# Kernel optimization log

Measured on AMD Instinct MI355X. Metric: run time of the kernel, lower is better.

Reference implementation:

```python
import jax, jax.numpy as jnp
import numpy as np

T, B, I, H, L = 512, 32, 512, 1024, 2


def setup_inputs() -> dict:
    key = jax.random.key(0)
    ks = jax.random.split(key, 10)
    std = 1.0 / np.sqrt(H)
    u = lambda k, shape: jax.random.uniform(k, shape, jnp.float32, -std, std)
    return {
        "x": jax.random.normal(ks[0], (T, B, I), jnp.float32),
        "Wxh0": u(ks[1], (4 * H, I)),
        "bxh0": u(ks[2], (4 * H,)),
        "Whh0": u(ks[3], (4 * H, H)),
        "bhh0": u(ks[4], (4 * H,)),
        "Wxh1": u(ks[5], (4 * H, H)),
        "bxh1": u(ks[6], (4 * H,)),
        "Whh1": u(ks[7], (4 * H, H)),
        "bhh1": u(ks[8], (4 * H,)),
    }


def _lstm_layer(x_seq, Wxh, bxh, Whh, bhh):
    # x_seq: (T, B, D_in). Precompute input projections for all timesteps.
    xg = jnp.einsum('tbi,gi->tbg', x_seq, Wxh) + bxh  # (T, B, 4H)
    h0 = jnp.zeros((x_seq.shape[1], H), x_seq.dtype)
    c0 = jnp.zeros_like(h0)

    def step(carry, xg_t):
        h, c = carry
        gates = xg_t + h @ Whh.T + bhh  # (B, 4H)
        i_g, f_g, g_g, o_g = jnp.split(gates, 4, axis=-1)
        c_new = jax.nn.sigmoid(f_g) * c + jax.nn.sigmoid(i_g) * jnp.tanh(g_g)
        h_new = jax.nn.sigmoid(o_g) * jnp.tanh(c_new)
        return (h_new, c_new), h_new

    (h_T, c_T), hs = jax.lax.scan(step, (h0, c0), xg)
    return hs, h_T, c_T  # hs: (T, B, H)


def reference(x, Wxh0, bxh0, Whh0, bhh0, Wxh1, bxh1, Whh1, bhh1):
    # Layer 0 consumes raw input; layer 1 consumes layer-0 hidden sequence.
    # Processing layer-by-layer is mathematically identical to the original
    # interleaved (t, layer) loop for a stacked unidirectional LSTM.
    hs0, h0T, c0T = _lstm_layer(x, Wxh0, bxh0, Whh0, bhh0)
    hs1, h1T, c1T = _lstm_layer(hs0, Wxh1, bxh1, Whh1, bhh1)
    output = hs1  # (T, B, H): hidden of last layer at each timestep
    h_n = jnp.stack([h0T, h1T])  # (L, B, H)
    c_n = jnp.stack([c0T, c1T])
    return output, h_n, c_n
```

## Files before the change

### kernel.cpp

```cpp
#include <hip/hip_runtime.h>


typedef unsigned short u16;
typedef __attribute__((ext_vector_type(8))) __bf16 bf16x8;
typedef __attribute__((ext_vector_type(8))) u16 u16x8;
typedef __attribute__((ext_vector_type(4))) float f32x4;
typedef __attribute__((ext_vector_type(2))) float f32x2;
typedef __attribute__((ext_vector_type(4))) int i32x4;
typedef __attribute__((ext_vector_type(4))) unsigned int u32x4;

#define HN_OFF 16777216
#define CN_OFF 16842752

__device__ __forceinline__ u16 f2bf(float f) {
  unsigned u = __builtin_bit_cast(unsigned, f);
  u += 0x7FFFu + ((u >> 16) & 1u);
  return (u16)(u >> 16);
}
__device__ __forceinline__ float sgm(float x) { return 1.f / (1.f + __expf(-x)); }
__device__ __forceinline__ float tnh(float x) { return 2.f / (1.f + __expf(-2.f * x)) - 1.f; }

__device__ __forceinline__ bf16x8 ld16(const u16* p) {
  u32x4 v = *reinterpret_cast<const u32x4*>(p);
  return __builtin_bit_cast(bf16x8, v);
}
__device__ __forceinline__ bf16x8 lds16(const char* p) {
  u32x4 v = *reinterpret_cast<const u32x4*>(p);
  return __builtin_bit_cast(bf16x8, v);
}
__device__ __forceinline__ f32x4 mfma16(bf16x8 a, bf16x8 b, f32x4 c) {
  return __builtin_amdgcn_mfma_f32_16x16x32_bf16(a, b, c, 0, 0, 0);
}

__device__ __forceinline__ void pollge(const int* flags, int lane, int s) {
  const int* p = flags + (lane << 2);
  for (;;) {
    i32x4 f;
    asm volatile("global_load_dwordx4 %0, %1, off sc0 sc1\n\ts_waitcnt vmcnt(0)"
                 : "=v"(f) : "v"(p) : "memory");
    if (__all((f[0] >= s) & (f[1] >= s) & (f[2] >= s) & (f[3] >= s))) break;
  }
}

template <int C0, int C1>
__device__ __forceinline__ void chunks_h0(const u16* __restrict__ A,
                                          const char* w0, const char* w1, int lane,
                                          f32x4& p0, f32x4& p1, f32x4& q0, f32x4& q1) {
  const int r = lane & 15, kq = (lane >> 4) * 8, swz = (r & 7) << 4;
#pragma unroll
  for (int c = C0; c < C1; ++c) {
    const u16* ap = A + r * 1024 + c * 32 + kq;
    bf16x8 a0 = ld16(ap);
    bf16x8 a1 = ld16(ap + 16 * 1024);
    bf16x8 b0 = lds16(w0 + r * 3072 + ((c * 64 + kq * 2) ^ swz));
    bf16x8 b1 = lds16(w1 + r * 4096 + (((c + 32) * 64 + kq * 2) ^ swz));
    p0 = mfma16(a0, b0, p0);  p1 = mfma16(a1, b0, p1);
    q0 = mfma16(a0, b1, q0);  q1 = mfma16(a1, b1, q1);
  }
}
template <int C0, int C1>
__device__ __forceinline__ void chunks_h1(const u16* __restrict__ A,
                                          const char* w1, int lane,
                                          f32x4& p0, f32x4& p1) {
  const int r = lane & 15, kq = (lane >> 4) * 8, swz = (r & 7) << 4;
#pragma unroll
  for (int c = C0; c < C1; ++c) {
    const u16* ap = A + r * 1024 + c * 32 + kq;
    bf16x8 a0 = ld16(ap);
    bf16x8 a1 = ld16(ap + 16 * 1024);
    bf16x8 bw = lds16(w1 + r * 4096 + ((c * 64 + kq * 2) ^ swz));
    p0 = mfma16(a0, bw, p0);  p1 = mfma16(a1, bw, p1);
  }
}
template <int C0, int C1>
__device__ __forceinline__ void chunks_x(const u16* __restrict__ A,
                                         const char* w0, int lane,
                                         f32x4& q0, f32x4& q1) {
  const int r = lane & 15, kq = (lane >> 4) * 8, swz = (r & 7) << 4;
#pragma unroll
  for (int c = C0; c < C1; ++c) {
    const u16* ap = A + r * 512 + c * 32 + kq;
    bf16x8 a0 = ld16(ap);
    bf16x8 a1 = ld16(ap + 16 * 512);
    bf16x8 bw = lds16(w0 + r * 3072 + (((c + 32) * 64 + kq * 2) ^ swz));
    q0 = mfma16(a0, bw, q0);  q1 = mfma16(a1, bw, q1);
  }
}

__global__ __launch_bounds__(512, 2) void lstm_fused(
    const u16* __restrict__ xbf,
    const float* __restrict__ Whh0, const float* __restrict__ Wxh0,
    const float* __restrict__ Whh1, const float* __restrict__ Wxh1,
    const float* __restrict__ bxh0, const float* __restrict__ bhh0,
    const float* __restrict__ bxh1, const float* __restrict__ bhh1,
    u16* __restrict__ h0seq, u16* __restrict__ h1seq,
    int* __restrict__ flag0, int* __restrict__ flag1,
    float* __restrict__ out) {
  extern __shared__ char smem[];
  const char* w0 = smem;
  const char* w1 = smem + 49152;
  auto part = reinterpret_cast<float(*)[32][18]>(smem + 114688);
  float* bias0 = reinterpret_cast<float*>(smem + 151552);
  float* bias1 = reinterpret_cast<float*>(smem + 151616);
  volatile int* go = reinterpret_cast<volatile int*>(smem + 151680);

  const int tid = threadIdx.x;
  const int wg = blockIdx.x;
  const int wid = tid >> 6, lane = tid & 63;

  if (tid == 0) { go[0] = 0; go[1] = 0; }
  for (int g = tid; g < 3072; g += 512) {
    int n = g / 192, gi = g % 192, kc = gi * 8;
    int gr = ((n >> 2) << 10) + (wg << 2) + (n & 3);
    const float* src = (kc < 1024) ? (Whh0 + gr * 1024 + kc) : (Wxh0 + gr * 512 + (kc - 1024));
    f32x4 lo = *reinterpret_cast<const f32x4*>(src);
    f32x4 hi = *reinterpret_cast<const f32x4*>(src + 4);
    u16x8 o;
    o[0]=f2bf(lo[0]); o[1]=f2bf(lo[1]); o[2]=f2bf(lo[2]); o[3]=f2bf(lo[3]);
    o[4]=f2bf(hi[0]); o[5]=f2bf(hi[1]); o[6]=f2bf(hi[2]); o[7]=f2bf(hi[3]);
    *reinterpret_cast<u16x8*>(smem + n * 3072 + ((gi * 16) ^ ((n & 7) << 4))) = o;
  }
  for (int g = tid; g < 4096; g += 512) {
    int n = g / 256, gi = g % 256, kc = gi * 8;
    int gr = ((n >> 2) << 10) + (wg << 2) + (n & 3);
    const float* src = (kc < 1024) ? (Whh1 + gr * 1024 + kc) : (Wxh1 + gr * 1024 + (kc - 1024));
    f32x4 lo = *reinterpret_cast<const f32x4*>(src);
    f32x4 hi = *reinterpret_cast<const f32x4*>(src + 4);
    u16x8 o;
    o[0]=f2bf(lo[0]); o[1]=f2bf(lo[1]); o[2]=f2bf(lo[2]); o[3]=f2bf(lo[3]);
    o[4]=f2bf(hi[0]); o[5]=f2bf(hi[1]); o[6]=f2bf(hi[2]); o[7]=f2bf(hi[3]);
    *reinterpret_cast<u16x8*>(smem + 49152 + n * 4096 + ((gi * 16) ^ ((n & 7) << 4))) = o;
  }
  if (tid < 16) {
    int gr = ((tid >> 2) << 10) + (wg << 2) + (tid & 3);
    bias0[tid] = bxh0[gr] + bhh0[gr];
    bias1[tid] = bxh1[gr] + bhh1[gr];
  }
  __syncthreads();

  float c0a = 0.f, c0b = 0.f, c1a = 0.f, c1b = 0.f;
  const int bg = lane >> 1, jjb = (lane & 1) << 1;
  const int colb = (wg << 2) + jjb;

  for (int s = 0; s <= 512; ++s) {
    const u16* h0slot = h0seq + s * 32768;
    const u16* h1prev = h1seq + (s - 1) * 32768;
    f32x4 p0 = {0,0,0,0}, p1 = {0,0,0,0}, q0 = {0,0,0,0}, q1 = {0,0,0,0};

    if (wid < 4) {
      if (s >= 1) {
        if (wid == 0) {
          pollge(flag0, lane, s);
          if (lane == 0) go[0] = s;
        } else {
          while (go[0] < s) __builtin_amdgcn_s_sleep(1);
        }
      }
      if      (wid == 0) chunks_h0<0,  8 >(h0slot, w0, w1, lane, p0, p1, q0, q1);
      else if (wid == 1) chunks_h0<8,  16>(h0slot, w0, w1, lane, p0, p1, q0, q1);
      else if (wid == 2) chunks_h0<16, 24>(h0slot, w0, w1, lane, p0, p1, q0, q1);
      else               chunks_h0<24, 32>(h0slot, w0, w1, lane, p0, p1, q0, q1);
    } else {
      const u16* xbt = xbf + s * 16384;
      if      (wid == 4) chunks_x<0,  4 >(xbt, w0, lane, q0, q1);
      else if (wid == 5) chunks_x<4,  8 >(xbt, w0, lane, q0, q1);
      else if (wid == 6) chunks_x<8,  12>(xbt, w0, lane, q0, q1);
      else               chunks_x<12, 16>(xbt, w0, lane, q0, q1);
      if (s >= 2) {
        if (wid == 4) {
          pollge(flag1, lane, s);
          if (lane == 0) go[1] = s;
        } else {
          while (go[1] < s) __builtin_amdgcn_s_sleep(1);
        }
      }
      if      (wid == 4) chunks_h1<0,  8 >(h1prev, w1, lane, p0, p1);
      else if (wid == 5) chunks_h1<8,  16>(h1prev, w1, lane, p0, p1);
      else if (wid == 6) chunks_h1<16, 24>(h1prev, w1, lane, p0, p1);
      else               chunks_h1<24, 32>(h1prev, w1, lane, p0, p1);
    }

    {
      const int n = lane & 15, br = (lane >> 4) * 4;
#pragma unroll
      for (int j = 0; j < 4; ++j) {
        part[wid][br + j][n]      = p0[j];
        part[wid][br + j + 16][n] = p1[j];
        part[8 + wid][br + j][n]      = q0[j];
        part[8 + wid][br + j + 16][n] = q1[j];
      }
    }
    __syncthreads();

    if (wid == 0) {
      if (s < 512) {
        float v[4][2];
#pragma unroll
        for (int gi = 0; gi < 4; ++gi) {
          const int n = (gi << 2) + jjb;
          float s0 = bias0[n], s1 = bias0[n + 1];
#pragma unroll
          for (int p = 0; p < 4; ++p) {
            f32x2 a = *reinterpret_cast<const f32x2*>(&part[p][bg][n]);
            f32x2 b = *reinterpret_cast<const f32x2*>(&part[12 + p][bg][n]);
            s0 += a[0] + b[0];  s1 += a[1] + b[1];
          }
          v[gi][0] = s0; v[gi][1] = s1;
        }
        c0a = sgm(v[1][0]) * c0a + sgm(v[0][0]) * tnh(v[2][0]);
        c0b = sgm(v[1][1]) * c0b + sgm(v[0][1]) * tnh(v[2][1]);
        const float ha = sgm(v[3][0]) * tnh(c0a), hb = sgm(v[3][1]) * tnh(c0b);
        unsigned pk = (unsigned)f2bf(ha) | ((unsigned)f2bf(hb) << 16);
        u16* hp = h0seq + (s + 1) * 32768 + bg * 1024 + colb;
        asm volatile("global_store_dword %0, %1, off sc0 sc1" :: "v"(hp), "v"(pk) : "memory");
        if (s == 511) {
          *reinterpret_cast<f32x2*>(out + HN_OFF + bg * 1024 + colb) = f32x2{ha, hb};
          *reinterpret_cast<f32x2*>(out + CN_OFF + bg * 1024 + colb) = f32x2{c0a, c0b};
        }
        asm volatile("s_waitcnt vmcnt(0)" ::: "memory");
        if (lane == 0) {
          int* fp = flag0 + wg;  int fv = s + 1;
          asm volatile("global_store_dword %0, %1, off sc0 sc1" :: "v"(fp), "v"(fv) : "memory");
        }
      }
    } else if (wid == 4) {
      if (s >= 1) {
        float v[4][2];
#pragma unroll
        for (int gi = 0; gi < 4; ++gi) {
          const int n = (gi << 2) + jjb;
          float s0 = bias1[n], s1 = bias1[n + 1];
#pragma unroll
          for (int p = 4; p < 12; ++p) {
            f32x2 a = *reinterpret_cast<const f32x2*>(&part[p][bg][n]);
            s0 += a[0];  s1 += a[1];
          }
          v[gi][0] = s0; v[gi][1] = s1;
        }
        c1a = sgm(v[1][0]) * c1a + sgm(v[0][0]) * tnh(v[2][0]);
        c1b = sgm(v[1][1]) * c1b + sgm(v[0][1]) * tnh(v[2][1]);
        const float ha = sgm(v[3][0]) * tnh(c1a), hb = sgm(v[3][1]) * tnh(c1b);
        unsigned pk = (unsigned)f2bf(ha) | ((unsigned)f2bf(hb) << 16);
        u16* hp = h1seq + s * 32768 + bg * 1024 + colb;
        asm volatile("global_store_dword %0, %1, off sc0 sc1" :: "v"(hp), "v"(pk) : "memory");
        const int t1 = s - 1;
        *reinterpret_cast<f32x2*>(out + t1 * 32768 + bg * 1024 + colb) = f32x2{ha, hb};
        if (t1 == 511) {
          *reinterpret_cast<f32x2*>(out + HN_OFF + 32768 + bg * 1024 + colb) = f32x2{ha, hb};
          *reinterpret_cast<f32x2*>(out + CN_OFF + 32768 + bg * 1024 + colb) = f32x2{c1a, c1b};
        }
        asm volatile("s_waitcnt vmcnt(0)" ::: "memory");
        if (lane == 0) {
          int* fp = flag1 + wg;  int fv = s + 1;
          asm volatile("global_store_dword %0, %1, off sc0 sc1" :: "v"(fp), "v"(fv) : "memory");
        }
      }
    }

    if (s == 512) break;
    __syncthreads();
  }
}

__global__ void cvt_bf16(const float* __restrict__ s, u16* __restrict__ d, int n) {
  int i = (blockIdx.x * blockDim.x + threadIdx.x) * 4;
  const int stride = gridDim.x * blockDim.x * 4;
  typedef __attribute__((ext_vector_type(4))) u16 u16x4;
  for (; i < n; i += stride) {
    f32x4 v = *reinterpret_cast<const f32x4*>(s + i);
    u16x4 o;
    o[0] = f2bf(v[0]); o[1] = f2bf(v[1]); o[2] = f2bf(v[2]); o[3] = f2bf(v[3]);
    *reinterpret_cast<u16x4*>(d + i) = o;
  }
}

extern "C" void kernel_launch(void* const* d_in, const int* in_sizes, int n_in,
                              void* d_out, int out_size, void* d_ws, size_t ws_size,
                              hipStream_t stream) {
  const float* x    = (const float*)d_in[0];
  const float* Wxh0 = (const float*)d_in[1];
  const float* bxh0 = (const float*)d_in[2];
  const float* Whh0 = (const float*)d_in[3];
  const float* bhh0 = (const float*)d_in[4];
  const float* Wxh1 = (const float*)d_in[5];
  const float* bxh1 = (const float*)d_in[6];
  const float* Whh1 = (const float*)d_in[7];
  const float* bhh1 = (const float*)d_in[8];
  char* ws = (char*)d_ws;
  u16* xbf   = (u16*)(ws);
  u16* h0seq = (u16*)(ws + 16777216);
  u16* h1seq = (u16*)(ws + 50397184);
  int* flag0 = (int*)(ws + 84017152);
  int* flag1 = (int*)(ws + 84018176);

  cvt_bf16<<<2048, 256, 0, stream>>>(x, xbf, 512 * 32 * 512);
  (void)hipMemsetAsync(h0seq, 0, 65536, stream);
  (void)hipMemsetAsync(h1seq, 0, 65536, stream);
  (void)hipMemsetAsync(flag0, 0, 2048, stream);

  (void)hipFuncSetAttribute(reinterpret_cast<const void*>(lstm_fused),
                            hipFuncAttributeMaxDynamicSharedMemorySize, 151744);
  lstm_fused<<<dim3(256), dim3(512), 151744, stream>>>(
      xbf, Whh0, Wxh0, Whh1, Wxh1, bxh0, bhh0, bxh1, bhh1,
      h0seq, h1seq, flag0, flag1, (float*)d_out);
}
```

Measured before the change: 3.437 ms.

## Merge per-layer grid flags into one epoch barrier with a single master poller

Replaces the two per-step flag polls (layer-0 waves and layer-1 waves each polling all 256 workgroup flags) with one combined barrier. Workgroup 0 polls both flag arrays and publishes an epoch word, and every other workgroup spins on that single dword. The input-projection MFMAs are hoisted ahead of the barrier so they overlap the wait. Cell-update duties move to waves 1 and 5, flag stores are issued before the output writes, and the trailing intra-block sync is dropped because the grid barrier now orders reuse of the shared partials. This cuts polling traffic on the flag lines, but it adds an extra hop of latency through the master workgroup and couples the two layers' progress at every step.

```diff
diff --git a/kernel.cpp b/kernel.cpp
--- a/kernel.cpp
+++ b/kernel.cpp
@@ -32,13 +32,25 @@
   return __builtin_amdgcn_mfma_f32_16x16x32_bf16(a, b, c, 0, 0, 0);
 }
 
-__device__ __forceinline__ void pollge(const int* flags, int lane, int s) {
-  const int* p = flags + (lane << 2);
+__device__ __forceinline__ void poll_flags(const int* f, int lane, int s) {
+  const int* p0 = f + (lane << 2);
+  const int* p1 = f + 256 + (lane << 2);
   for (;;) {
-    i32x4 f;
-    asm volatile("global_load_dwordx4 %0, %1, off sc0 sc1\n\ts_waitcnt vmcnt(0)"
-                 : "=v"(f) : "v"(p) : "memory");
-    if (__all((f[0] >= s) & (f[1] >= s) & (f[2] >= s) & (f[3] >= s))) break;
+    i32x4 a, b;
+    asm volatile("global_load_dwordx4 %0, %2, off sc0 sc1\n\t"
+                 "global_load_dwordx4 %1, %3, off sc0 sc1\n\t"
+                 "s_waitcnt vmcnt(0)"
+                 : "=v"(a), "=v"(b) : "v"(p0), "v"(p1) : "memory");
+    if (__all((a[0] >= s) & (a[1] >= s) & (a[2] >= s) & (a[3] >= s) &
+              (b[0] >= s) & (b[1] >= s) & (b[2] >= s) & (b[3] >= s))) break;
+  }
+}
+__device__ __forceinline__ void poll_epoch(const int* ep, int s) {
+  for (;;) {
+    int e;
+    asm volatile("global_load_dword %0, %1, off sc0 sc1\n\ts_waitcnt vmcnt(0)"
+                 : "=v"(e) : "v"(ep) : "memory");
+    if (e >= s) break;
   }
 }
 
@@ -94,7 +106,7 @@
     const float* __restrict__ bxh0, const float* __restrict__ bhh0,
     const float* __restrict__ bxh1, const float* __restrict__ bhh1,
     u16* __restrict__ h0seq, u16* __restrict__ h1seq,
-    int* __restrict__ flag0, int* __restrict__ flag1,
+    int* __restrict__ flagbase,
     float* __restrict__ out) {
   extern __shared__ char smem[];
   const char* w0 = smem;
@@ -104,11 +116,15 @@
   float* bias1 = reinterpret_cast<float*>(smem + 151616);
   volatile int* go = reinterpret_cast<volatile int*>(smem + 151680);
 
+  int* flag0 = flagbase;
+  int* flag1 = flagbase + 256;
+  int* epoch = flagbase + 512;
+
   const int tid = threadIdx.x;
   const int wg = blockIdx.x;
   const int wid = tid >> 6, lane = tid & 63;
 
-  if (tid == 0) { go[0] = 0; go[1] = 0; }
+  if (tid == 0) go[0] = 0;
   for (int g = tid; g < 3072; g += 512) {
     int n = g / 192, gi = g % 192, kc = gi * 8;
     int gr = ((n >> 2) << 10) + (wg << 2) + (n & 3);
@@ -147,33 +163,38 @@
     const u16* h1prev = h1seq + (s - 1) * 32768;
     f32x4 p0 = {0,0,0,0}, p1 = {0,0,0,0}, q0 = {0,0,0,0}, q1 = {0,0,0,0};
 
-    if (wid < 4) {
-      if (s >= 1) {
-        if (wid == 0) {
-          pollge(flag0, lane, s);
-          if (lane == 0) go[0] = s;
-        } else {
-          while (go[0] < s) __builtin_amdgcn_s_sleep(1);
-        }
-      }
-      if      (wid == 0) chunks_h0<0,  8 >(h0slot, w0, w1, lane, p0, p1, q0, q1);
-      else if (wid == 1) chunks_h0<8,  16>(h0slot, w0, w1, lane, p0, p1, q0, q1);
-      else if (wid == 2) chunks_h0<16, 24>(h0slot, w0, w1, lane, p0, p1, q0, q1);
-      else               chunks_h0<24, 32>(h0slot, w0, w1, lane, p0, p1, q0, q1);
-    } else {
+    if (wid >= 4 && s < 512) {
       const u16* xbt = xbf + s * 16384;
       if      (wid == 4) chunks_x<0,  4 >(xbt, w0, lane, q0, q1);
       else if (wid == 5) chunks_x<4,  8 >(xbt, w0, lane, q0, q1);
       else if (wid == 6) chunks_x<8,  12>(xbt, w0, lane, q0, q1);
       else               chunks_x<12, 16>(xbt, w0, lane, q0, q1);
-      if (s >= 2) {
-        if (wid == 4) {
-          pollge(flag1, lane, s);
-          if (lane == 0) go[1] = s;
+    }
+
+    if (s >= 1) {
+      if (wid == 0) {
+        if (wg == 0) {
+          poll_flags(flag0, lane, s);
+          if (lane == 0) {
+            int sv = s;
+            asm volatile("global_store_dword %0, %1, off sc0 sc1"
+                         :: "v"(epoch), "v"(sv) : "memory");
+          }
         } else {
-          while (go[1] < s) __builtin_amdgcn_s_sleep(1);
-        }
+          poll_epoch(epoch, s);
+        }
+        if (lane == 0) go[0] = s;
+      } else {
+        while (go[0] < s) __builtin_amdgcn_s_sleep(1);
       }
+    }
+
+    if (wid < 4) {
+      if      (wid == 0) chunks_h0<0,  8 >(h0slot, w0, w1, lane, p0, p1, q0, q1);
+      else if (wid == 1) chunks_h0<8,  16>(h0slot, w0, w1, lane, p0, p1, q0, q1);
+      else if (wid == 2) chunks_h0<16, 24>(h0slot, w0, w1, lane, p0, p1, q0, q1);
+      else               chunks_h0<24, 32>(h0slot, w0, w1, lane, p0, p1, q0, q1);
+    } else if (s >= 1) {
       if      (wid == 4) chunks_h1<0,  8 >(h1prev, w1, lane, p0, p1);
       else if (wid == 5) chunks_h1<8,  16>(h1prev, w1, lane, p0, p1);
       else if (wid == 6) chunks_h1<16, 24>(h1prev, w1, lane, p0, p1);
@@ -184,15 +205,15 @@
       const int n = lane & 15, br = (lane >> 4) * 4;
 #pragma unroll
       for (int j = 0; j < 4; ++j) {
-        part[wid][br + j][n]      = p0[j];
-        part[wid][br + j + 16][n] = p1[j];
+        part[wid][br + j][n]          = p0[j];
+        part[wid][br + j + 16][n]     = p1[j];
         part[8 + wid][br + j][n]      = q0[j];
         part[8 + wid][br + j + 16][n] = q1[j];
       }
     }
     __syncthreads();
 
-    if (wid == 0) {
+    if (wid == 1) {
       if (s < 512) {
         float v[4][2];
 #pragma unroll
@@ -213,17 +234,17 @@
         unsigned pk = (unsigned)f2bf(ha) | ((unsigned)f2bf(hb) << 16);
         u16* hp = h0seq + (s + 1) * 32768 + bg * 1024 + colb;
         asm volatile("global_store_dword %0, %1, off sc0 sc1" :: "v"(hp), "v"(pk) : "memory");
-        if (s == 511) {
-          *reinterpret_cast<f32x2*>(out + HN_OFF + bg * 1024 + colb) = f32x2{ha, hb};
-          *reinterpret_cast<f32x2*>(out + CN_OFF + bg * 1024 + colb) = f32x2{c0a, c0b};
-        }
         asm volatile("s_waitcnt vmcnt(0)" ::: "memory");
         if (lane == 0) {
           int* fp = flag0 + wg;  int fv = s + 1;
           asm volatile("global_store_dword %0, %1, off sc0 sc1" :: "v"(fp), "v"(fv) : "memory");
         }
+        if (s == 511) {
+          *reinterpret_cast<f32x2*>(out + HN_OFF + bg * 1024 + colb) = f32x2{ha, hb};
+          *reinterpret_cast<f32x2*>(out + CN_OFF + bg * 1024 + colb) = f32x2{c0a, c0b};
+        }
       }
-    } else if (wid == 4) {
+    } else if (wid == 5) {
       if (s >= 1) {
         float v[4][2];
 #pragma unroll
@@ -243,22 +264,22 @@
         unsigned pk = (unsigned)f2bf(ha) | ((unsigned)f2bf(hb) << 16);
         u16* hp = h1seq + s * 32768 + bg * 1024 + colb;
         asm volatile("global_store_dword %0, %1, off sc0 sc1" :: "v"(hp), "v"(pk) : "memory");
+        asm volatile("s_waitcnt vmcnt(0)" ::: "memory");
+        if (lane == 0) {
+          int* fp = flag1 + wg;  int fv = s + 1;
+          asm volatile("global_store_dword %0, %1, off sc0 sc1" :: "v"(fp), "v"(fv) : "memory");
+        }
         const int t1 = s - 1;
         *reinterpret_cast<f32x2*>(out + t1 * 32768 + bg * 1024 + colb) = f32x2{ha, hb};
         if (t1 == 511) {
           *reinterpret_cast<f32x2*>(out + HN_OFF + 32768 + bg * 1024 + colb) = f32x2{ha, hb};
           *reinterpret_cast<f32x2*>(out + CN_OFF + 32768 + bg * 1024 + colb) = f32x2{c1a, c1b};
         }
-        asm volatile("s_waitcnt vmcnt(0)" ::: "memory");
-        if (lane == 0) {
-          int* fp = flag1 + wg;  int fv = s + 1;
-          asm volatile("global_store_dword %0, %1, off sc0 sc1" :: "v"(fp), "v"(fv) : "memory");
-        }
+      } else if (lane == 0) {
+        int* fp = flag1 + wg;  int fv = 1;
+        asm volatile("global_store_dword %0, %1, off sc0 sc1" :: "v"(fp), "v"(fv) : "memory");
       }
     }
-
-    if (s == 512) break;
-    __syncthreads();
   }
 }
 
@@ -287,20 +308,19 @@
   const float* Whh1 = (const float*)d_in[7];
   const float* bhh1 = (const float*)d_in[8];
   char* ws = (char*)d_ws;
-  u16* xbf   = (u16*)(ws);
-  u16* h0seq = (u16*)(ws + 16777216);
-  u16* h1seq = (u16*)(ws + 50397184);
-  int* flag0 = (int*)(ws + 84017152);
-  int* flag1 = (int*)(ws + 84018176);
+  u16* xbf      = (u16*)(ws);
+  u16* h0seq    = (u16*)(ws + 16777216);
+  u16* h1seq    = (u16*)(ws + 50397184);
+  int* flagbase = (int*)(ws + 84017152);
 
   cvt_bf16<<<2048, 256, 0, stream>>>(x, xbf, 512 * 32 * 512);
   (void)hipMemsetAsync(h0seq, 0, 65536, stream);
   (void)hipMemsetAsync(h1seq, 0, 65536, stream);
-  (void)hipMemsetAsync(flag0, 0, 2048, stream);
+  (void)hipMemsetAsync(flagbase, 0, 4096, stream);
 
   (void)hipFuncSetAttribute(reinterpret_cast<const void*>(lstm_fused),
                             hipFuncAttributeMaxDynamicSharedMemorySize, 151744);
   lstm_fused<<<dim3(256), dim3(512), 151744, stream>>>(
       xbf, Whh0, Wxh0, Whh1, Wxh1, bxh0, bhh0, bxh1, bhh1,
-      h0seq, h1seq, flag0, flag1, (float*)d_out);
-}
+      h0seq, h1seq, flagbase, (float*)d_out);
+}
```

Result: slower. 3.517 ms (+2.3%).

## Replace flag polling with sentinel-filled hidden-state buffers and prefetch x projections

Applied to the files above, without the earlier changes.

Each step's hidden-state buffer is pre-filled with a 0xFFFFFFFF sentinel, and consumer waves poll the data itself (16 dwordx4 loads per lane, retried until no sentinel remains). This removes the separate flag arrays, the store-then-wait-then-flag round trip on the producer side, and the LDS 'go' broadcast. The x-input projection for step s+1 is now computed by spare waves after the gate stage of step s, taking it off the critical path, and gate finalisation moves to waves 1 and 5. The price is a 64 MB sentinel memset per call and wider polling loads, and correctness relies on real bf16 outputs never matching the sentinel.

```diff
diff --git a/kernel.cpp b/kernel.cpp
--- a/kernel.cpp
+++ b/kernel.cpp
@@ -6,11 +6,11 @@
 typedef __attribute__((ext_vector_type(8))) u16 u16x8;
 typedef __attribute__((ext_vector_type(4))) float f32x4;
 typedef __attribute__((ext_vector_type(2))) float f32x2;
-typedef __attribute__((ext_vector_type(4))) int i32x4;
 typedef __attribute__((ext_vector_type(4))) unsigned int u32x4;
 
 #define HN_OFF 16777216
 #define CN_OFF 16842752
+#define SENTU 0xFFFFFFFFu
 
 __device__ __forceinline__ u16 f2bf(float f) {
   unsigned u = __builtin_bit_cast(unsigned, f);
@@ -32,46 +32,46 @@
   return __builtin_amdgcn_mfma_f32_16x16x32_bf16(a, b, c, 0, 0, 0);
 }
 
-__device__ __forceinline__ void pollge(const int* flags, int lane, int s) {
-  const int* p = flags + (lane << 2);
-  for (;;) {
-    i32x4 f;
-    asm volatile("global_load_dwordx4 %0, %1, off sc0 sc1\n\ts_waitcnt vmcnt(0)"
-                 : "=v"(f) : "v"(p) : "memory");
-    if (__all((f[0] >= s) & (f[1] >= s) & (f[2] >= s) & (f[3] >= s))) break;
-  }
-}
-
-template <int C0, int C1>
-__device__ __forceinline__ void chunks_h0(const u16* __restrict__ A,
-                                          const char* w0, const char* w1, int lane,
-                                          f32x4& p0, f32x4& p1, f32x4& q0, f32x4& q1) {
-  const int r = lane & 15, kq = (lane >> 4) * 8, swz = (r & 7) << 4;
-#pragma unroll
-  for (int c = C0; c < C1; ++c) {
-    const u16* ap = A + r * 1024 + c * 32 + kq;
-    bf16x8 a0 = ld16(ap);
-    bf16x8 a1 = ld16(ap + 16 * 1024);
-    bf16x8 b0 = lds16(w0 + r * 3072 + ((c * 64 + kq * 2) ^ swz));
-    bf16x8 b1 = lds16(w1 + r * 4096 + (((c + 32) * 64 + kq * 2) ^ swz));
-    p0 = mfma16(a0, b0, p0);  p1 = mfma16(a1, b0, p1);
-    q0 = mfma16(a0, b1, q0);  q1 = mfma16(a1, b1, q1);
-  }
-}
-template <int C0, int C1>
-__device__ __forceinline__ void chunks_h1(const u16* __restrict__ A,
-                                          const char* w1, int lane,
-                                          f32x4& p0, f32x4& p1) {
-  const int r = lane & 15, kq = (lane >> 4) * 8, swz = (r & 7) << 4;
-#pragma unroll
-  for (int c = C0; c < C1; ++c) {
-    const u16* ap = A + r * 1024 + c * 32 + kq;
-    bf16x8 a0 = ld16(ap);
-    bf16x8 a1 = ld16(ap + 16 * 1024);
-    bf16x8 bw = lds16(w1 + r * 4096 + ((c * 64 + kq * 2) ^ swz));
-    p0 = mfma16(a0, bw, p0);  p1 = mfma16(a1, bw, p1);
-  }
-}
+#define LD8A(a,b,c,d_,e,f,g,h,off,bs)                                   \
+  asm volatile("global_load_dwordx4 %0, %8, %9 offset:0 sc0 sc1\n\t"    \
+               "global_load_dwordx4 %1, %8, %9 offset:64 sc0 sc1\n\t"   \
+               "global_load_dwordx4 %2, %8, %9 offset:128 sc0 sc1\n\t"  \
+               "global_load_dwordx4 %3, %8, %9 offset:192 sc0 sc1\n\t"  \
+               "global_load_dwordx4 %4, %8, %9 offset:256 sc0 sc1\n\t"  \
+               "global_load_dwordx4 %5, %8, %9 offset:320 sc0 sc1\n\t"  \
+               "global_load_dwordx4 %6, %8, %9 offset:384 sc0 sc1\n\t"  \
+               "global_load_dwordx4 %7, %8, %9 offset:448 sc0 sc1"      \
+               : "=&v"(a), "=&v"(b), "=&v"(c), "=&v"(d_), "=&v"(e),     \
+                 "=&v"(f), "=&v"(g), "=&v"(h)                           \
+               : "v"(off), "s"(bs) : "memory")
+
+#define DECL16 u32x4 d0,d1,d2,d3,d4,d5,d6,d7,d8,d9,d10,d11,d12,d13,d14,d15
+#define CHK(v) (((v)[0]==SENTU)|((v)[1]==SENTU)|((v)[2]==SENTU)|((v)[3]==SENTU))
+#define RETRY16(bs,o0,o1)                                                   \
+  for (;;) {                                                                \
+    LD8A(d0,d1,d2,d3,d4,d5,d6,d7,(o0),(bs));                                \
+    LD8A(d8,d9,d10,d11,d12,d13,d14,d15,(o1),(bs));                          \
+    asm volatile("s_waitcnt vmcnt(0)" ::: "memory");                        \
+    __builtin_amdgcn_sched_barrier(0);                                      \
+    unsigned bad = CHK(d0)|CHK(d1)|CHK(d2)|CHK(d3)|CHK(d4)|CHK(d5)|CHK(d6)  \
+                 |CHK(d7)|CHK(d8)|CHK(d9)|CHK(d10)|CHK(d11)|CHK(d12)        \
+                 |CHK(d13)|CHK(d14)|CHK(d15);                               \
+    if (!__any(bad)) break;                                                 \
+    __builtin_amdgcn_s_sleep(1);                                            \
+  }
+
+#define MM_L0(di,dj,c) {                                                    \
+    bf16x8 b0 = lds16(w0 + r*3072 + (((c)*64 + kq2) ^ swz));                \
+    bf16x8 b1 = lds16(w1 + r*4096 + ((((c)+32)*64 + kq2) ^ swz));           \
+    bf16x8 a0 = __builtin_bit_cast(bf16x8, di);                             \
+    bf16x8 a1 = __builtin_bit_cast(bf16x8, dj);                             \
+    p0 = mfma16(a0,b0,p0);  p1 = mfma16(a1,b0,p1);                          \
+    qa = mfma16(a0,b1,qa);  qb = mfma16(a1,b1,qb); }
+#define MM_L1(di,dj,c) {                                                    \
+    bf16x8 bw = lds16(w1 + r*4096 + (((c)*64 + kq2) ^ swz));                \
+    p0 = mfma16(__builtin_bit_cast(bf16x8, di), bw, p0);                    \
+    p1 = mfma16(__builtin_bit_cast(bf16x8, dj), bw, p1); }
+
 template <int C0, int C1>
 __device__ __forceinline__ void chunks_x(const u16* __restrict__ A,
                                          const char* w0, int lane,
@@ -94,7 +94,6 @@
     const float* __restrict__ bxh0, const float* __restrict__ bhh0,
     const float* __restrict__ bxh1, const float* __restrict__ bhh1,
     u16* __restrict__ h0seq, u16* __restrict__ h1seq,
-    int* __restrict__ flag0, int* __restrict__ flag1,
     float* __restrict__ out) {
   extern __shared__ char smem[];
   const char* w0 = smem;
@@ -102,13 +101,12 @@
   auto part = reinterpret_cast<float(*)[32][18]>(smem + 114688);
   float* bias0 = reinterpret_cast<float*>(smem + 151552);
   float* bias1 = reinterpret_cast<float*>(smem + 151616);
-  volatile int* go = reinterpret_cast<volatile int*>(smem + 151680);
 
   const int tid = threadIdx.x;
   const int wg = blockIdx.x;
   const int wid = tid >> 6, lane = tid & 63;
-
-  if (tid == 0) { go[0] = 0; go[1] = 0; }
+  const int r = lane & 15, kq2 = ((lane >> 4) << 3) * 2, swz = (r & 7) << 4;
+
   for (int g = tid; g < 3072; g += 512) {
     int n = g / 192, gi = g % 192, kc = gi * 8;
     int gr = ((n >> 2) << 10) + (wg << 2) + (n & 3);
@@ -142,57 +140,53 @@
   const int bg = lane >> 1, jjb = (lane & 1) << 1;
   const int colb = (wg << 2) + jjb;
 
+  f32x4 xq0 = {0,0,0,0}, xq1 = {0,0,0,0};
+  if      (wid == 4) chunks_x<0, 6 >(xbf, w0, lane, xq0, xq1);
+  else if (wid == 6) chunks_x<6, 11>(xbf, w0, lane, xq0, xq1);
+  else if (wid == 7) chunks_x<11,16>(xbf, w0, lane, xq0, xq1);
+
   for (int s = 0; s <= 512; ++s) {
-    const u16* h0slot = h0seq + s * 32768;
-    const u16* h1prev = h1seq + (s - 1) * 32768;
-    f32x4 p0 = {0,0,0,0}, p1 = {0,0,0,0}, q0 = {0,0,0,0}, q1 = {0,0,0,0};
+    f32x4 p0 = {0,0,0,0}, p1 = {0,0,0,0}, qa = {0,0,0,0}, qb = {0,0,0,0};
 
     if (wid < 4) {
-      if (s >= 1) {
-        if (wid == 0) {
-          pollge(flag0, lane, s);
-          if (lane == 0) go[0] = s;
-        } else {
-          while (go[0] < s) __builtin_amdgcn_s_sleep(1);
-        }
-      }
-      if      (wid == 0) chunks_h0<0,  8 >(h0slot, w0, w1, lane, p0, p1, q0, q1);
-      else if (wid == 1) chunks_h0<8,  16>(h0slot, w0, w1, lane, p0, p1, q0, q1);
-      else if (wid == 2) chunks_h0<16, 24>(h0slot, w0, w1, lane, p0, p1, q0, q1);
-      else               chunks_h0<24, 32>(h0slot, w0, w1, lane, p0, p1, q0, q1);
-    } else {
-      const u16* xbt = xbf + s * 16384;
-      if      (wid == 4) chunks_x<0,  4 >(xbt, w0, lane, q0, q1);
-      else if (wid == 5) chunks_x<4,  8 >(xbt, w0, lane, q0, q1);
-      else if (wid == 6) chunks_x<8,  12>(xbt, w0, lane, q0, q1);
-      else               chunks_x<12, 16>(xbt, w0, lane, q0, q1);
-      if (s >= 2) {
-        if (wid == 4) {
-          pollge(flag1, lane, s);
-          if (lane == 0) go[1] = s;
-        } else {
-          while (go[1] < s) __builtin_amdgcn_s_sleep(1);
-        }
-      }
-      if      (wid == 4) chunks_h1<0,  8 >(h1prev, w1, lane, p0, p1);
-      else if (wid == 5) chunks_h1<8,  16>(h1prev, w1, lane, p0, p1);
-      else if (wid == 6) chunks_h1<16, 24>(h1prev, w1, lane, p0, p1);
-      else               chunks_h1<24, 32>(h1prev, w1, lane, p0, p1);
+      const u16* hb = h0seq + (size_t)s * 32768;
+      const int off0 = r * 2048 + wid * 512 + kq2;
+      const int off1 = off0 + 32768;
+      DECL16;
+      RETRY16(hb, off0, off1);
+      const int c0 = wid * 8;
+      MM_L0(d0, d8,  c0 + 0); MM_L0(d1, d9,  c0 + 1);
+      MM_L0(d2, d10, c0 + 2); MM_L0(d3, d11, c0 + 3);
+      MM_L0(d4, d12, c0 + 4); MM_L0(d5, d13, c0 + 5);
+      MM_L0(d6, d14, c0 + 6); MM_L0(d7, d15, c0 + 7);
+    } else if (s >= 1) {
+      const u16* hb = h1seq + (size_t)(s - 1) * 32768;
+      const int off0 = r * 2048 + (wid - 4) * 512 + kq2;
+      const int off1 = off0 + 32768;
+      DECL16;
+      RETRY16(hb, off0, off1);
+      const int c0 = (wid - 4) * 8;
+      MM_L1(d0, d8,  c0 + 0); MM_L1(d1, d9,  c0 + 1);
+      MM_L1(d2, d10, c0 + 2); MM_L1(d3, d11, c0 + 3);
+      MM_L1(d4, d12, c0 + 4); MM_L1(d5, d13, c0 + 5);
+      MM_L1(d6, d14, c0 + 6); MM_L1(d7, d15, c0 + 7);
     }
 
     {
       const int n = lane & 15, br = (lane >> 4) * 4;
+      const f32x4 q0 = (wid < 4) ? qa : xq0;
+      const f32x4 q1 = (wid < 4) ? qb : xq1;
 #pragma unroll
       for (int j = 0; j < 4; ++j) {
-        part[wid][br + j][n]      = p0[j];
-        part[wid][br + j + 16][n] = p1[j];
+        part[wid][br + j][n]          = p0[j];
+        part[wid][br + j + 16][n]     = p1[j];
         part[8 + wid][br + j][n]      = q0[j];
         part[8 + wid][br + j + 16][n] = q1[j];
       }
     }
     __syncthreads();
 
-    if (wid == 0) {
+    if (wid == 1) {
       if (s < 512) {
         float v[4][2];
 #pragma unroll
@@ -211,19 +205,14 @@
         c0b = sgm(v[1][1]) * c0b + sgm(v[0][1]) * tnh(v[2][1]);
         const float ha = sgm(v[3][0]) * tnh(c0a), hb = sgm(v[3][1]) * tnh(c0b);
         unsigned pk = (unsigned)f2bf(ha) | ((unsigned)f2bf(hb) << 16);
-        u16* hp = h0seq + (s + 1) * 32768 + bg * 1024 + colb;
+        u16* hp = h0seq + (size_t)(s + 1) * 32768 + bg * 1024 + colb;
         asm volatile("global_store_dword %0, %1, off sc0 sc1" :: "v"(hp), "v"(pk) : "memory");
         if (s == 511) {
           *reinterpret_cast<f32x2*>(out + HN_OFF + bg * 1024 + colb) = f32x2{ha, hb};
           *reinterpret_cast<f32x2*>(out + CN_OFF + bg * 1024 + colb) = f32x2{c0a, c0b};
         }
-        asm volatile("s_waitcnt vmcnt(0)" ::: "memory");
-        if (lane == 0) {
-          int* fp = flag0 + wg;  int fv = s + 1;
-          asm volatile("global_store_dword %0, %1, off sc0 sc1" :: "v"(fp), "v"(fv) : "memory");
-        }
       }
-    } else if (wid == 4) {
+    } else if (wid == 5) {
       if (s >= 1) {
         float v[4][2];
 #pragma unroll
@@ -241,7 +230,7 @@
         c1b = sgm(v[1][1]) * c1b + sgm(v[0][1]) * tnh(v[2][1]);
         const float ha = sgm(v[3][0]) * tnh(c1a), hb = sgm(v[3][1]) * tnh(c1b);
         unsigned pk = (unsigned)f2bf(ha) | ((unsigned)f2bf(hb) << 16);
-        u16* hp = h1seq + s * 32768 + bg * 1024 + colb;
+        u16* hp = h1seq + (size_t)s * 32768 + bg * 1024 + colb;
         asm volatile("global_store_dword %0, %1, off sc0 sc1" :: "v"(hp), "v"(pk) : "memory");
         const int t1 = s - 1;
         *reinterpret_cast<f32x2*>(out + t1 * 32768 + bg * 1024 + colb) = f32x2{ha, hb};
@@ -249,12 +238,16 @@
           *reinterpret_cast<f32x2*>(out + HN_OFF + 32768 + bg * 1024 + colb) = f32x2{ha, hb};
           *reinterpret_cast<f32x2*>(out + CN_OFF + 32768 + bg * 1024 + colb) = f32x2{c1a, c1b};
         }
-        asm volatile("s_waitcnt vmcnt(0)" ::: "memory");
-        if (lane == 0) {
-          int* fp = flag1 + wg;  int fv = s + 1;
-          asm volatile("global_store_dword %0, %1, off sc0 sc1" :: "v"(fp), "v"(fv) : "memory");
-        }
       }
+    } else if (wid == 4 && s < 511) {
+      xq0 = f32x4{0,0,0,0}; xq1 = f32x4{0,0,0,0};
+      chunks_x<0, 6>(xbf + (size_t)(s + 1) * 16384, w0, lane, xq0, xq1);
+    } else if (wid == 6 && s < 511) {
+      xq0 = f32x4{0,0,0,0}; xq1 = f32x4{0,0,0,0};
+      chunks_x<6, 11>(xbf + (size_t)(s + 1) * 16384, w0, lane, xq0, xq1);
+    } else if (wid == 7 && s < 511) {
+      xq0 = f32x4{0,0,0,0}; xq1 = f32x4{0,0,0,0};
+      chunks_x<11, 16>(xbf + (size_t)(s + 1) * 16384, w0, lane, xq0, xq1);
     }
 
     if (s == 512) break;
@@ -290,17 +283,16 @@
   u16* xbf   = (u16*)(ws);
   u16* h0seq = (u16*)(ws + 16777216);
   u16* h1seq = (u16*)(ws + 50397184);
-  int* flag0 = (int*)(ws + 84017152);
-  int* flag1 = (int*)(ws + 84018176);
 
   cvt_bf16<<<2048, 256, 0, stream>>>(x, xbf, 512 * 32 * 512);
   (void)hipMemsetAsync(h0seq, 0, 65536, stream);
+  (void)hipMemsetAsync((char*)h0seq + 65536, 0xFF, 512 * 65536, stream);
   (void)hipMemsetAsync(h1seq, 0, 65536, stream);
-  (void)hipMemsetAsync(flag0, 0, 2048, stream);
+  (void)hipMemsetAsync((char*)h1seq + 65536, 0xFF, 512 * 65536, stream);
 
   (void)hipFuncSetAttribute(reinterpret_cast<const void*>(lstm_fused),
-                            hipFuncAttributeMaxDynamicSharedMemorySize, 151744);
-  lstm_fused<<<dim3(256), dim3(512), 151744, stream>>>(
+                            hipFuncAttributeMaxDynamicSharedMemorySize, 151680);
+  lstm_fused<<<dim3(256), dim3(512), 151680, stream>>>(
       xbf, Whh0, Wxh0, Whh1, Wxh1, bxh0, bhh0, bxh1, bhh1,
-      h0seq, h1seq, flag0, flag1, (float*)d_out);
-}
+      h0seq, h1seq, (float*)d_out);
+}
```

Result: slower. 4.397 ms (+27.9%).
